# Kernel tuning notes

Hardware: AMD Instinct MI355X
Metric: run time of the kernel (lower is better)

## Reference

```python
import jax, jax.numpy as jnp
import numpy as np

B, N, K, C_IN, D = 4, 2048, 16, 480, 64
EPS = 1e-5


def _c1(x, w, b):
    # 1x1 Conv1d: x (B,C,N), w (O,C) -> (B,O,N)
    return jnp.einsum('oc,bcn->bon', w, x) + b[:, None]


def _c2(x, w, b):
    # 1x1 Conv2d: x (B,C,J,N), w (O,C) -> (B,O,J,N)
    return jnp.einsum('oc,bcjn->bojn', w, x) + b[:, None, None]


def _bn(x, g, b):
    # eval-mode BatchNorm2d with running_mean=0, running_var=1
    return x * (g / jnp.sqrt(1.0 + EPS))[:, None, None] + b[:, None, None]


def _mlp_res(x, w1, b1, w2, b2, ws, bs):
    return _c1(jax.nn.relu(_c1(x, w1, b1)), w2, b2) + _c1(x, ws, bs)


def _group(f, idx):
    # f (B,C,N), idx (B,K,N) int -> out[b,c,j,n] = f[b,c,idx[b,j,n]]  -> (B,C,K,N)
    return jax.vmap(lambda ff, ii: ff[:, ii])(f, idx)


def _knn_idx(xyz):
    # xyz (B,3,N) -> idx (B,K,N), excluding the self point (nearest neighbor)
    pts = xyz.transpose(0, 2, 1)  # (B,N,3)
    sq = jnp.sum(pts * pts, -1)
    d2 = sq[:, :, None] + sq[:, None, :] - 2.0 * jnp.einsum('bnd,bmd->bnm', pts, pts)
    _, idx = jax.lax.top_k(-d2, K + 1)  # (B,N,K+1), nearest first
    return idx.transpose(0, 2, 1)[:, 1:, :]  # drop self -> (B,K,N)


def _forward(idx, feature, xyz, bt1_w, bt1_b, bt2_w, bt2_b, bts_w, bts_b,
             q_w, q_b, k_w, k_b, v_w, v_b,
             fd1_w, fd1_b, fd_g, fd_bb, fd2_w, fd2_b,
             fg1_w, fg1_b, fg_g, fg_bb, fg2_w, fg2_b,
             at_w, at_b, m41_w, m41_b, m42_w, m42_b):
    x = _mlp_res(feature, bt1_w, bt1_b, bt2_w, bt2_b, bts_w, bts_b)  # (B,64,N)
    q = _c1(x, q_w, q_b)
    k = _c1(x, k_w, k_b)
    v = _c1(x, v_w, v_b)

    group_xyz = _group(xyz, idx)                       # (B,3,K,N)
    rel_xyz = xyz[:, :, None, :] - group_xyz           # (B,3,K,N)
    pos_enc = _c2(jax.nn.relu(_bn(_c2(rel_xyz, fd1_w, fd1_b), fd_g, fd_bb)), fd2_w, fd2_b)  # (B,64,K,N)

    k_local = _group(k, idx)                           # (B,64,K,N)
    v_local = _group(v, idx)
    qk_rel = q[:, :, None, :] - k_local
    attn = _c2(jax.nn.relu(_bn(_c2(qk_rel + pos_enc, fg1_w, fg1_b), fg_g, fg_bb)), fg2_w, fg2_b)  # (B,64,K,N)

    attn1 = attn.transpose(0, 1, 3, 2)                 # (B,64,N,K)
    # ConvTranspose2d(64,64,(4,1),(4,1)) with kernel==stride: out[b,o,4n+r,f] = sum_c x[b,c,n,f]*W[c,o,r] + bias[o]
    y = jnp.einsum('bcnf,cor->bonrf', attn1, at_w)
    y = y.reshape(y.shape[0], y.shape[1], -1, y.shape[4]) + at_b[None, :, None, None]  # (B,64,4N,K)
    attn = jax.nn.softmax(y, axis=1)

    value_rel = (v_local + pos_enc).transpose(0, 1, 3, 2)   # (B,64,N,K)
    value = jnp.repeat(value_rel, 4, axis=2)                # nearest upsample (4,1) -> (B,64,4N,K)

    res = jnp.einsum('bmnf,bmnf->bmn', attn, value)         # (B,64,4N)
    identity = jnp.repeat(x, 4, axis=2)                     # nearest upsample x4 -> (B,64,4N)
    res = res + identity
    completion = _c1(jax.nn.relu(_c1(res, m41_w, m41_b)), m42_w, m42_b)  # (B,3,4N)
    return completion, res


def setup_inputs() -> dict:
    key = jax.random.key(0)
    ks = jax.random.split(key, 24)
    i = iter(range(24))

    def w(shape):
        return (jax.random.normal(ks[next(i)], shape, dtype=jnp.float32) * 0.05)

    z = lambda n: jnp.zeros((n,), jnp.float32)
    o = lambda n: jnp.ones((n,), jnp.float32)
    return {
        'feature': jax.random.normal(ks[next(i)], (B, C_IN, N), dtype=jnp.float32),
        'xyz': jax.random.normal(ks[next(i)], (B, 3, N), dtype=jnp.float32),
        'bt1_w': w((D, C_IN)), 'bt1_b': z(D),
        'bt2_w': w((D, D)), 'bt2_b': z(D),
        'bts_w': w((D, C_IN)), 'bts_b': z(D),
        'q_w': w((D, D)), 'q_b': z(D),
        'k_w': w((D, D)), 'k_b': z(D),
        'v_w': w((D, D)), 'v_b': z(D),
        'fd1_w': w((D, 3)), 'fd1_b': z(D), 'fd_g': o(D), 'fd_bb': z(D),
        'fd2_w': w((D, D)), 'fd2_b': z(D),
        'fg1_w': w((4 * D, D)), 'fg1_b': z(4 * D), 'fg_g': o(4 * D), 'fg_bb': z(4 * D),
        'fg2_w': w((D, 4 * D)), 'fg2_b': z(D),
        'at_w': w((D, D, 4)), 'at_b': z(D),
        'm41_w': w((D, D)), 'm41_b': z(D),
        'm42_w': w((3, D)), 'm42_b': z(3),
    }


def reference(feature, xyz, bt1_w, bt1_b, bt2_w, bt2_b, bts_w, bts_b,
              q_w, q_b, k_w, k_b, v_w, v_b,
              fd1_w, fd1_b, fd_g, fd_bb, fd2_w, fd2_b,
              fg1_w, fg1_b, fg_g, fg_bb, fg2_w, fg2_b,
              at_w, at_b, m41_w, m41_b, m42_w, m42_b):
    idx = _knn_idx(xyz)
    return _forward(idx, feature, xyz, bt1_w, bt1_b, bt2_w, bt2_b, bts_w, bts_b,
                    q_w, q_b, k_w, k_b, v_w, v_b,
                    fd1_w, fd1_b, fd_g, fd_bb, fd2_w, fd2_b,
                    fg1_w, fg1_b, fg_g, fg_bb, fg2_w, fg2_b,
                    at_w, at_b, m41_w, m41_b, m42_w, m42_b)
```

## Files before the change

### kernel.cpp

```cpp
#include <hip/hip_runtime.h>

#define B_ 4
#define N_ 2048
#define K_ 16
#define CIN_ 480
#define UPN_ 8192
#define M_ (B_*N_*K_)
#define MX_ (B_*N_)
#define KCAP 448

typedef unsigned int u32;
typedef unsigned short u16;
typedef unsigned long long u64;
typedef __attribute__((ext_vector_type(8))) short short8;
typedef __attribute__((ext_vector_type(4))) float f32x4;

#define DEV static __device__ __forceinline__

DEV float b2f(u16 h){ return __uint_as_float(((u32)h)<<16); }
DEV u16 f2b(float f){
  u32 u = __float_as_uint(f);
  u32 r = u + 0x7fffu + ((u>>16)&1u);
  return (u16)(r>>16);
}
DEV u32 pack2(float a, float b){ return (u32)f2b(a) | ((u32)f2b(b)<<16); }
DEV bool detect_bf(const void* fg){ return ((((const u32*)fg)[0]) & 0xFFFFu) == 0x3F80u; }
DEV float ld(const void* p, int i, bool bf){
  return bf ? b2f(((const u16*)p)[i]) : ((const float*)p)[i];
}
DEV u64 makekey(float d2, int m){
  u32 bits = __float_as_uint(d2);
  bits = (bits & 0x80000000u) ? ~bits : (bits | 0x80000000u);
  return ((u64)bits<<32) | (u32)m;
}
DEV int swz64(int row, int colByte){ return row*128 + (colByte ^ ((row&7)<<4)); }
DEV int swzH (int row, int colByte){ return row*512 + (colByte ^ ((row&7)<<4)); }

__global__ __launch_bounds__(256) void convert_kernel(const void* __restrict__ xyz,
    const void* __restrict__ fg, float* __restrict__ fxyz)
{
  bool bf = detect_bf(fg);
  const int XT = B_*3*N_;
  for(int i = blockIdx.x*256+threadIdx.x; i < XT; i += gridDim.x*256)
    fxyz[i] = bf ? b2f(((const u16*)xyz)[i]) : ((const float*)xyz)[i];
}

__global__ __launch_bounds__(256) void transpose_kernel(const void* __restrict__ feature,
    const void* __restrict__ fg, u16* __restrict__ fxbT)
{
  __shared__ u16 s[32][34];
  bool bf = detect_bf(fg);
  int ntile = blockIdx.x, ctile = blockIdx.y, b = blockIdx.z;
  int tx = threadIdx.x & 31, ty = threadIdx.x >> 5;
  u64 base = (u64)b*CIN_*N_;
  #pragma unroll
  for(int r=0;r<4;r++){
    int c = ctile*32 + ty + r*8;
    int n = ntile*32 + tx;
    u64 i = base + (u64)c*N_ + n;
    s[ty + r*8][tx] = bf ? ((const u16*)feature)[i] : f2b(((const float*)feature)[i]);
  }
  __syncthreads();
  #pragma unroll
  for(int r=0;r<4;r++){
    int nl = ty + r*8;
    int n = ntile*32 + nl;
    fxbT[(u64)b*N_*CIN_ + (u64)n*CIN_ + ctile*32 + tx] = s[tx][nl];
  }
}

__global__ __launch_bounds__(256) void prep_kernel(
    const void* __restrict__ bt1_w, const void* __restrict__ bt1_b,
    const void* __restrict__ bt2_w, const void* __restrict__ bt2_b,
    const void* __restrict__ bts_w, const void* __restrict__ bts_b,
    const void* __restrict__ q_w, const void* __restrict__ q_b,
    const void* __restrict__ k_w, const void* __restrict__ k_b,
    const void* __restrict__ v_w, const void* __restrict__ v_b,
    const void* __restrict__ fd1_w, const void* __restrict__ fd1_b,
    const void* __restrict__ fd_g, const void* __restrict__ fd_bb,
    const void* __restrict__ fd2_w, const void* __restrict__ fd2_b,
    const void* __restrict__ fg1_w, const void* __restrict__ fg1_b,
    const void* __restrict__ fg_g, const void* __restrict__ fg_bb,
    const void* __restrict__ fg2_w, const void* __restrict__ fg2_b,
    const void* __restrict__ at_w, const void* __restrict__ at_b,
    const void* __restrict__ m41_w, const void* __restrict__ m41_b,
    const void* __restrict__ m42_w, const void* __restrict__ m42_b,
    float* __restrict__ W, u16* __restrict__ WB)
{
  int t = blockIdx.x*256 + threadIdx.x;
  bool bf = detect_bf(fd_g);
  const float inv = 0.9999950000374997f;
  if(t < 30720){ int c=t>>6, o=t&63; W[t] = ld(bt1_w,o*CIN_+c,bf); return; } t -= 30720;
  if(t < 30720){ int c=t>>6, o=t&63; W[30720+t] = ld(bts_w,o*CIN_+c,bf); return; } t -= 30720;
  if(t < 4096){ int c=t>>6, o=t&63; W[61440+t] = ld(bt2_w,o*64+c,bf); return; } t -= 4096;
  if(t < 4096){ int c=t>>6, o=t&63; W[65536+t] = ld(q_w,o*64+c,bf); return; } t -= 4096;
  if(t < 4096){ int c=t>>6, o=t&63; W[69632+t] = ld(k_w,o*64+c,bf); return; } t -= 4096;
  if(t < 4096){ int c=t>>6, o=t&63; W[73728+t] = ld(v_w,o*64+c,bf); return; } t -= 4096;
  if(t < 256){
    int o=t>>2, j=t&3; float s = ld(fd_g,o,bf)*inv;
    W[77824+t] = (j<3) ? s*ld(fd1_w,o*3+j,bf) : (s*ld(fd1_b,o,bf) + ld(fd_bb,o,bf));
    return;
  } t -= 256;
  if(t < 4096){ int o=t>>6, m=t&63; W[78080+t] = ld(fd2_w,m*64+o,bf); return; } t -= 4096;
  if(t < 16384){ int o=t>>6; float s=ld(fg_g,o,bf)*inv; W[82176+t] = s*ld(fg1_w,t,bf); return; } t -= 16384;
  if(t < 256){ float s=ld(fg_g,t,bf)*inv; W[98560+t] = s*ld(fg1_b,t,bf) + ld(fg_bb,t,bf); return; } t -= 256;
  if(t < 16384){ int o=t>>6, m=t&63; W[98816+t] = ld(fg2_w,m*256+o,bf); return; } t -= 16384;
  if(t < 16384){ int r=t>>12, rem=t&4095, o=rem>>6, c=rem&63;
                 W[115200+t] = ld(at_w,(c*64+o)*4+r,bf); return; } t -= 16384;
  if(t < 4096){ int m=t>>6, o=t&63; W[131584+t] = ld(m41_w,o*64+m,bf); return; } t -= 4096;
  if(t < 192){ W[135680+t] = ld(m42_w,t,bf); return; } t -= 192;
  if(t < 64){ W[135872+t] = ld(bt1_b,t,bf); return; } t -= 64;
  if(t < 64){ W[135936+t] = ld(bts_b,t,bf); return; } t -= 64;
  if(t < 64){ W[136000+t] = ld(bt2_b,t,bf); return; } t -= 64;
  if(t < 64){ W[136064+t] = ld(q_b,t,bf); return; } t -= 64;
  if(t < 64){ W[136128+t] = ld(k_b,t,bf); return; } t -= 64;
  if(t < 64){ W[136192+t] = ld(v_b,t,bf); return; } t -= 64;
  if(t < 64){ W[136256+t] = ld(fd2_b,t,bf); return; } t -= 64;
  if(t < 64){ W[136320+t] = ld(fg2_b,t,bf); return; } t -= 64;
  if(t < 64){ W[136384+t] = ld(at_b,t,bf); return; } t -= 64;
  if(t < 64){ W[136448+t] = ld(m41_b,t,bf); return; } t -= 64;
  if(t < 3){ W[136512+t] = ld(m42_b,t,bf); return; } t -= 3;
  if(t < 16384){ int o=t>>6; float s=ld(fg_g,o,bf)*inv; WB[t] = f2b(s*ld(fg1_w,t,bf)); return; } t -= 16384;
  if(t < 16384){ WB[16384+t] = f2b(ld(fg2_w,t,bf)); return; } t -= 16384;
  if(t < 16384){ int j=t>>6, c=t&63;
                 WB[32768+t] = f2b(ld(at_w,(c*64+(j&63))*4+(j>>6),bf)); return; } t -= 16384;
  if(t < 256){ W[136576+t] = ld(at_b,t&63,bf); return; } t -= 256;
  if(t < 4096){ WB[49152+t] = f2b(ld(fd2_w,t,bf)); return; } t -= 4096;
  if(t < 30720){ WB[53248+t] = f2b(ld(bt1_w,t,bf)); return; } t -= 30720;
  if(t < 30720){ WB[83968+t] = f2b(ld(bts_w,t,bf)); return; } t -= 30720;
  if(t < 4096){ WB[114688+t] = f2b(ld(bt2_w,t,bf)); return; } t -= 4096;
  if(t < 4096){ WB[118784+t] = f2b(ld(q_w,t,bf)); return; } t -= 4096;
  if(t < 4096){ WB[122880+t] = f2b(ld(k_w,t,bf)); return; } t -= 4096;
  if(t < 4096){ WB[126976+t] = f2b(ld(v_w,t,bf)); return; }
}

__global__ __launch_bounds__(256) void knn_kernel(const float* __restrict__ fxyz,
                                                  int* __restrict__ idx)
{
  __shared__ float px[N_], py[N_], pz[N_], sq[N_];
  __shared__ u64 sbuf[4][KCAP];
  __shared__ u64 smin[4][64];
  __shared__ int scnt[4][64];
  __shared__ u64 stau[4];
  int b = blockIdx.y;
  const float* xb = fxyz + (u64)b*3*N_;
  for(int i=threadIdx.x;i<N_;i+=256){
    float xx=xb[i], yy=xb[N_+i], zz=xb[2*N_+i];
    px[i]=xx; py[i]=yy; pz[i]=zz; sq[i]=xx*xx+yy*yy+zz*zz;
  }
  __syncthreads();
  int w = threadIdx.x>>6, l = threadIdx.x&63;
  int q = blockIdx.x*4 + w;
  float qx=px[q], qy=py[q], qz=pz[q], qs=sq[q];
  float d2c[32];
  u64 best=~0ull;
  #pragma unroll
  for(int j=0;j<32;j++){
    int m = l*32 + ((j+l)&31);
    float d2 = (qs+sq[m]) - 2.0f*(qx*px[m]+qy*py[m]+qz*pz[m]);
    d2c[j]=d2;
    u64 key = makekey(d2, m);
    best = key<best ? key : best;
  }
  smin[w][l]=best;
  __syncthreads();
  {
    int rank=0;
    for(int i=0;i<64;i++) rank += (smin[w][i] < best);
    if(rank==16) stau[w] = best;
  }
  __syncthreads();
  u64 tau = stau[w];
  int myc=0;
  #pragma unroll
  for(int j=0;j<32;j++){
    int m = l*32 + ((j+l)&31);
    myc += (makekey(d2c[j], m) <= tau);
  }
  scnt[w][l]=myc;
  __syncthreads();
  int off=0, tot=0;
  for(int i=0;i<64;i++){
    int c = scnt[w][i];
    tot += c;
    off += (i<l) ? c : 0;
  }
  #pragma unroll
  for(int j=0;j<32;j++){
    int m = l*32 + ((j+l)&31);
    u64 key = makekey(d2c[j], m);
    if(key<=tau && off<KCAP){ sbuf[w][off]=key; off++; }
  }
  __syncthreads();
  if(tot>KCAP) tot=KCAP;
  for(int p=l; p<tot; p+=64){
    u64 kk = sbuf[w][p];
    int rk=0;
    for(int i=0;i<tot;i++) rk += (sbuf[w][i] < kk);
    if(rk>=1 && rk<17) idx[(b*K_+(rk-1))*N_+q] = ((int)(kk & 0xffffffffu)) & (N_-1);
  }
}

__global__ __launch_bounds__(256) void gemm480_mfma(const u16* __restrict__ A,
    const u16* __restrict__ Wt, const float* __restrict__ bias,
    u16* __restrict__ hout, float* __restrict__ xsout)
{
  int tid=threadIdx.x, w=tid>>6, lane=tid&63;
  int rbase=(blockIdx.x*4+w)*64;
  int cbase=blockIdx.y*64;
  int lr=lane&15, lk=(lane>>4)*8;
  f32x4 acc[4][4];
  #pragma unroll
  for(int i=0;i<4;i++)
    #pragma unroll
    for(int j=0;j<4;j++) acc[i][j]=(f32x4){0.f,0.f,0.f,0.f};
  for(int kc=0;kc<CIN_;kc+=32){
    short8 a[4], bb[4];
    #pragma unroll
    for(int ti=0;ti<4;ti++)
      a[ti] = *(const short8*)(A + (u64)(rbase+ti*16+lr)*CIN_ + kc + lk);
    #pragma unroll
    for(int tj=0;tj<4;tj++)
      bb[tj] = *(const short8*)(Wt + (u64)(cbase+tj*16+lr)*CIN_ + kc + lk);
    #pragma unroll
    for(int ti=0;ti<4;ti++)
      #pragma unroll
      for(int tj=0;tj<4;tj++)
        acc[ti][tj] = __builtin_amdgcn_mfma_f32_16x16x32_bf16(a[ti], bb[tj], acc[ti][tj], 0,0,0);
  }
  int rq=(lane>>4)*4;
  #pragma unroll
  for(int ti=0;ti<4;ti++)
    #pragma unroll
    for(int tj=0;tj<4;tj++){
      int col = cbase + tj*16 + lr;
      float bv = bias[col];
      #pragma unroll
      for(int reg=0;reg<4;reg++){
        u64 row = rbase + ti*16 + rq + reg;
        float vv = acc[ti][tj][reg] + bv;
        if(blockIdx.y==0) hout[row*64 + col] = f2b(fmaxf(vv,0.f));
        else              xsout[row*64 + (col-64)] = vv;
      }
    }
}

__global__ __launch_bounds__(256) void x_mfma(const u16* __restrict__ A,
    const u16* __restrict__ Wt, const float* __restrict__ bias,
    const float* __restrict__ xs, float* __restrict__ x, u16* __restrict__ xb)
{
  int tid=threadIdx.x, w=tid>>6, lane=tid&63;
  int rbase=(blockIdx.x*4+w)*64;
  int lr=lane&15, lk=(lane>>4)*8;
  f32x4 acc[4][4];
  #pragma unroll
  for(int i=0;i<4;i++)
    #pragma unroll
    for(int j=0;j<4;j++) acc[i][j]=(f32x4){0.f,0.f,0.f,0.f};
  for(int kc=0;kc<64;kc+=32){
    short8 a[4], bb[4];
    #pragma unroll
    for(int ti=0;ti<4;ti++)
      a[ti] = *(const short8*)(A + (u64)(rbase+ti*16+lr)*64 + kc + lk);
    #pragma unroll
    for(int tj=0;tj<4;tj++)
      bb[tj] = *(const short8*)(Wt + (u64)(tj*16+lr)*64 + kc + lk);
    #pragma unroll
    for(int ti=0;ti<4;ti++)
      #pragma unroll
      for(int tj=0;tj<4;tj++)
        acc[ti][tj] = __builtin_amdgcn_mfma_f32_16x16x32_bf16(a[ti], bb[tj], acc[ti][tj], 0,0,0);
  }
  int rq=(lane>>4)*4;
  #pragma unroll
  for(int ti=0;ti<4;ti++)
    #pragma unroll
    for(int tj=0;tj<4;tj++){
      int col = tj*16 + lr;
      float bv = bias[col];
      #pragma unroll
      for(int reg=0;reg<4;reg++){
        u64 row = rbase + ti*16 + rq + reg;
        float vv = acc[ti][tj][reg] + bv + xs[row*64+col];
        x[row*64+col] = vv;
        xb[row*64+col] = f2b(vv);
      }
    }
}

__global__ __launch_bounds__(256) void qkv_mfma(const u16* __restrict__ A,
    const u16* __restrict__ Wt, const float* __restrict__ bias, float* __restrict__ qkv)
{
  int tid=threadIdx.x, w=tid>>6, lane=tid&63;
  int rbase=(blockIdx.x*4+w)*64;
  int cbase=blockIdx.y*64;
  int lr=lane&15, lk=(lane>>4)*8;
  f32x4 acc[4][4];
  #pragma unroll
  for(int i=0;i<4;i++)
    #pragma unroll
    for(int j=0;j<4;j++) acc[i][j]=(f32x4){0.f,0.f,0.f,0.f};
  for(int kc=0;kc<64;kc+=32){
    short8 a[4], bb[4];
    #pragma unroll
    for(int ti=0;ti<4;ti++)
      a[ti] = *(const short8*)(A + (u64)(rbase+ti*16+lr)*64 + kc + lk);
    #pragma unroll
    for(int tj=0;tj<4;tj++)
      bb[tj] = *(const short8*)(Wt + (u64)(cbase+tj*16+lr)*64 + kc + lk);
    #pragma unroll
    for(int ti=0;ti<4;ti++)
      #pragma unroll
      for(int tj=0;tj<4;tj++)
        acc[ti][tj] = __builtin_amdgcn_mfma_f32_16x16x32_bf16(a[ti], bb[tj], acc[ti][tj], 0,0,0);
  }
  int rq=(lane>>4)*4;
  #pragma unroll
  for(int ti=0;ti<4;ti++)
    #pragma unroll
    for(int tj=0;tj<4;tj++){
      int col = cbase + tj*16 + lr;
      float bv = bias[col];
      #pragma unroll
      for(int reg=0;reg<4;reg++){
        u64 row = rbase + ti*16 + rq + reg;
        qkv[row*192 + col] = acc[ti][tj][reg] + bv;
      }
    }
}

__global__ __launch_bounds__(256) void fused_chain(
    const int* __restrict__ idx, const float* __restrict__ fxyz,
    const float* __restrict__ qkv, const float* __restrict__ x,
    const float* __restrict__ fd1f,
    const u16* __restrict__ Wfd2, const float* __restrict__ bfd2,
    const u16* __restrict__ Wfg1, const float* __restrict__ bfg1,
    const u16* __restrict__ Wfg2, const float* __restrict__ bfg2,
    const u16* __restrict__ Wat,  const float* __restrict__ bat,
    const void* __restrict__ det, void* __restrict__ out)
{
  __shared__ alignas(16) unsigned char lds[49152];
  int tid = threadIdx.x;
  int w = tid>>6, lane = tid&63;
  int lr = lane&15, lk = (lane>>4)*8, rq = (lane>>4)*4;

  int erow = tid>>2, ecg = tid&3;
  int el = erow>>4, ef = erow&15;
  int bn_e = blockIdx.x*4 + el;
  int b_e = bn_e>>11, n_e = bn_e&(N_-1);
  int jn = idx[(b_e*K_+ef)*N_ + n_e] & (N_-1);

  {
    const float* xb = fxyz + (u64)b_e*3*N_;
    float rx = xb[n_e]      - xb[jn];
    float ry = xb[N_+n_e]   - xb[N_+jn];
    float rz = xb[2*N_+n_e] - xb[2*N_+jn];
    #pragma unroll
    for(int gg=0; gg<4; gg++){
      u64 pk=0;
      #pragma unroll
      for(int j=0;j<4;j++){
        f32x4 wv = *(const f32x4*)(fd1f + ((ecg*4+gg)*4+j)*4);
        float tv = fmaxf(wv[0]*rx + wv[1]*ry + wv[2]*rz + wv[3], 0.f);
        pk |= (u64)f2b(tv) << (16*j);
      }
      *(u64*)(lds + swz64(erow, (ecg*4+gg)*8)) = pk;
    }
  }
  __syncthreads();

  {
    f32x4 acc[4];
    #pragma unroll
    for(int i=0;i<4;i++) acc[i]=(f32x4){0.f,0.f,0.f,0.f};
    #pragma unroll
    for(int kc=0;kc<64;kc+=32){
      short8 wf = *(const short8*)(Wfd2 + (u64)(w*16+lr)*64 + kc + lk);
      #pragma unroll
      for(int ti=0;ti<4;ti++){
        short8 tf = *(const short8*)(lds + swz64(ti*16+lr, (kc+lk)*2));
        acc[ti] = __builtin_amdgcn_mfma_f32_16x16x32_bf16(wf, tf, acc[ti], 0,0,0);
      }
    }
    f32x4 b4 = *(const f32x4*)(bfd2 + w*16 + rq);
    #pragma unroll
    for(int ti=0;ti<4;ti++){
      u64 pk=0;
      #pragma unroll
      for(int reg=0;reg<4;reg++) pk |= (u64)f2b(acc[ti][reg] + b4[reg]) << (16*reg);
      *(u64*)(lds + 8192 + swz64(ti*16+lr, (w*16+rq)*2)) = pk;
    }
  }
  __syncthreads();

  {
    int mg = ecg*16;
    const float* qrow = qkv + (u64)(b_e*N_+n_e)*192 + mg;
    const float* krow = qkv + (u64)(b_e*N_+jn)*192 + 64 + mg;
    const float* vrow = qkv + (u64)(b_e*N_+jn)*192 + 128 + mg;
    #pragma unroll
    for(int g2=0; g2<4; g2++){
      f32x4 qv = *(const f32x4*)(qrow + g2*4);
      f32x4 kv = *(const f32x4*)(krow + g2*4);
      f32x4 vv = *(const f32x4*)(vrow + g2*4);
      int cb = (mg + g2*4)*2;
      u64 pw = *(const u64*)(lds + 8192 + swz64(erow, cb));
      u64 aw=0, vw=0;
      #pragma unroll
      for(int j=0;j<4;j++){
        float pv = b2f((u16)(pw>>(16*j)));
        aw |= (u64)f2b(qv[j] - kv[j] + pv) << (16*j);
        vw |= (u64)f2b(vv[j] + pv) << (16*j);
      }
      *(u64*)(lds + swz64(erow, cb)) = aw;
      *(u64*)(lds + 8192 + swz64(erow, cb)) = vw;
    }
  }
  __syncthreads();

  {
    f32x4 acc[4][4];
    #pragma unroll
    for(int i=0;i<4;i++)
      #pragma unroll
      for(int j=0;j<4;j++) acc[i][j]=(f32x4){0.f,0.f,0.f,0.f};
    #pragma unroll
    for(int kc=0;kc<64;kc+=32){
      short8 wf[4], af[4];
      #pragma unroll
      for(int ti=0;ti<4;ti++)
        wf[ti] = *(const short8*)(Wfg1 + (u64)(w*64+ti*16+lr)*64 + kc + lk);
      #pragma unroll
      for(int tj=0;tj<4;tj++)
        af[tj] = *(const short8*)(lds + swz64(tj*16+lr, (kc+lk)*2));
      #pragma unroll
      for(int ti=0;ti<4;ti++)
        #pragma unroll
        for(int tj=0;tj<4;tj++)
          acc[ti][tj] = __builtin_amdgcn_mfma_f32_16x16x32_bf16(wf[ti], af[tj], acc[ti][tj], 0,0,0);
    }
    #pragma unroll
    for(int ti=0;ti<4;ti++){
      f32x4 b4 = *(const f32x4*)(bfg1 + w*64 + ti*16 + rq);
      #pragma unroll
      for(int tj=0;tj<4;tj++){
        int rowh = tj*16 + lr;
        u64 pk=0;
        #pragma unroll
        for(int reg=0;reg<4;reg++)
          pk |= (u64)f2b(fmaxf(acc[ti][tj][reg] + b4[reg], 0.f)) << (16*reg);
        *(u64*)(lds + 16384 + swzH(rowh, (w*64+ti*16+rq)*2)) = pk;
      }
    }
  }
  __syncthreads();

  {
    f32x4 acc[4];
    #pragma unroll
    for(int i=0;i<4;i++) acc[i]=(f32x4){0.f,0.f,0.f,0.f};
    #pragma unroll
    for(int kc=0;kc<256;kc+=32){
      short8 wf = *(const short8*)(Wfg2 + (u64)(w*16+lr)*256 + kc + lk);
      #pragma unroll
      for(int ti=0;ti<4;ti++){
        short8 hf = *(const short8*)(lds + 16384 + swzH(ti*16+lr, (kc+lk)*2));
        acc[ti] = __builtin_amdgcn_mfma_f32_16x16x32_bf16(wf, hf, acc[ti], 0,0,0);
      }
    }
    f32x4 b4 = *(const f32x4*)(bfg2 + w*16 + rq);
    #pragma unroll
    for(int ti=0;ti<4;ti++){
      u64 pk=0;
      #pragma unroll
      for(int reg=0;reg<4;reg++) pk |= (u64)f2b(acc[ti][reg] + b4[reg]) << (16*reg);
      *(u64*)(lds + swz64(ti*16+lr, (w*16+rq)*2)) = pk;
    }
  }
  __syncthreads();

  {
    f32x4 acc[4][4];
    #pragma unroll
    for(int i=0;i<4;i++)
      #pragma unroll
      for(int j=0;j<4;j++) acc[i][j]=(f32x4){0.f,0.f,0.f,0.f};
    #pragma unroll
    for(int kc=0;kc<64;kc+=32){
      short8 wf[4], gf[4];
      #pragma unroll
      for(int ti=0;ti<4;ti++)
        wf[ti] = *(const short8*)(Wat + (u64)(w*64+ti*16+lr)*64 + kc + lk);
      #pragma unroll
      for(int tj=0;tj<4;tj++)
        gf[tj] = *(const short8*)(lds + swz64(tj*16+lr, (kc+lk)*2));
      #pragma unroll
      for(int ti=0;ti<4;ti++)
        #pragma unroll
        for(int tj=0;tj<4;tj++)
          acc[ti][tj] = __builtin_amdgcn_mfma_f32_16x16x32_bf16(wf[ti], gf[tj], acc[ti][tj], 0,0,0);
    }
    #pragma unroll
    for(int ti=0;ti<4;ti++){
      f32x4 b4 = *(const f32x4*)(bat + w*64 + ti*16 + rq);
      #pragma unroll
      for(int tj=0;tj<4;tj++){
        int rowy = tj*16 + lr;
        u64 pk=0;
        #pragma unroll
        for(int reg=0;reg<4;reg++)
          pk |= (u64)f2b(acc[ti][tj][reg] + b4[reg]) << (16*reg);
        *(u64*)(lds + 16384 + swzH(rowy, (w*64+ti*16+rq)*2)) = pk;
      }
    }
  }
  __syncthreads();

  int f = lane>>2, r = lane&3;
  int rowl = w*16 + f;
  float yv[64];
  #pragma unroll
  for(int j=0;j<8;j++){
    uint4 pk = *(const uint4*)(lds + 16384 + swzH(rowl, r*128 + j*16));
    yv[j*8+0]=__uint_as_float(pk.x<<16); yv[j*8+1]=__uint_as_float(pk.x&0xffff0000u);
    yv[j*8+2]=__uint_as_float(pk.y<<16); yv[j*8+3]=__uint_as_float(pk.y&0xffff0000u);
    yv[j*8+4]=__uint_as_float(pk.z<<16); yv[j*8+5]=__uint_as_float(pk.z&0xffff0000u);
    yv[j*8+6]=__uint_as_float(pk.w<<16); yv[j*8+7]=__uint_as_float(pk.w&0xffff0000u);
  }
  __syncthreads();

  float mx = yv[0];
  #pragma unroll
  for(int m=1;m<64;m++) mx = fmaxf(mx, yv[m]);
  float sm = 0.f;
  #pragma unroll
  for(int m=0;m<64;m++){ float e = __expf(yv[m]-mx); yv[m]=e; sm+=e; }
  float rinv = 1.0f/sm;
  #pragma unroll
  for(int j=0;j<8;j++){
    uint4 pk;
    pk.x = pack2(yv[j*8+0]*rinv, yv[j*8+1]*rinv);
    pk.y = pack2(yv[j*8+2]*rinv, yv[j*8+3]*rinv);
    pk.z = pack2(yv[j*8+4]*rinv, yv[j*8+5]*rinv);
    pk.w = pack2(yv[j*8+6]*rinv, yv[j*8+7]*rinv);
    *(uint4*)(lds + 16384 + swz64(tid, j*16)) = pk;
  }
  __syncthreads();

  int m = lane;
  float a0=0.f,a1=0.f,a2=0.f,a3=0.f;
  #pragma unroll
  for(int f2=0; f2<16; f2++){
    float vvf = b2f(*(const u16*)(lds + 8192 + swz64(w*16+f2, m*2)));
    int spr = w*64 + f2*4;
    a0 += b2f(*(const u16*)(lds + 16384 + swz64(spr+0, m*2))) * vvf;
    a1 += b2f(*(const u16*)(lds + 16384 + swz64(spr+1, m*2))) * vvf;
    a2 += b2f(*(const u16*)(lds + 16384 + swz64(spr+2, m*2))) * vvf;
    a3 += b2f(*(const u16*)(lds + 16384 + swz64(spr+3, m*2))) * vvf;
  }
  int bn = blockIdx.x*4 + w;
  int b = bn>>11, n = bn&(N_-1);
  float xv = x[(u64)bn*64 + m];
  u64 off = 98304 + ((u64)(b*64+m))*UPN_ + (u64)n*4;
  if(detect_bf(det)){
    u64 pk = (u64)f2b(a0+xv) | ((u64)f2b(a1+xv)<<16)
           | ((u64)f2b(a2+xv)<<32) | ((u64)f2b(a3+xv)<<48);
    *(u64*)((u16*)out + off) = pk;
  } else {
    f32x4 pk = {a0+xv, a1+xv, a2+xv, a3+xv};
    *(f32x4*)((float*)out + off) = pk;
  }
}

__global__ __launch_bounds__(256) void comp_kernel(
  const float* __restrict__ m41T, const float* __restrict__ m41b,
  const float* __restrict__ m42f, const float* __restrict__ m42b,
  const void* __restrict__ det, void* __restrict__ out)
{
  int t = blockIdx.x*256 + threadIdx.x;
  int un = t & (UPN_-1);
  int b = t >> 13;
  bool bf = detect_bf(det);
  float acc[64];
  #pragma unroll
  for(int o=0;o<64;o++) acc[o] = m41b[o];
  if(bf){
    const u16* rr = (const u16*)out + 98304 + (u64)b*64*UPN_ + un;
    for(int c=0;c<64;c++){
      float rv = b2f(rr[(u64)c*UPN_]);
      const float* w = m41T + c*64;
      #pragma unroll
      for(int o=0;o<64;o++) acc[o] += w[o]*rv;
    }
  } else {
    const float* rr = (const float*)out + 98304 + (u64)b*64*UPN_ + un;
    for(int c=0;c<64;c++){
      float rv = rr[(u64)c*UPN_];
      const float* w = m41T + c*64;
      #pragma unroll
      for(int o=0;o<64;o++) acc[o] += w[o]*rv;
    }
  }
  float c0=m42b[0], c1=m42b[1], c2=m42b[2];
  #pragma unroll
  for(int o=0;o<64;o++){
    float hv = fmaxf(acc[o],0.f);
    c0 += m42f[o]*hv; c1 += m42f[64+o]*hv; c2 += m42f[128+o]*hv;
  }
  u64 base = (u64)b*3*UPN_ + un;
  if(bf){
    u16* cp = (u16*)out;
    cp[base]=f2b(c0); cp[base+UPN_]=f2b(c1); cp[base+2*UPN_]=f2b(c2);
  } else {
    float* cp = (float*)out;
    cp[base]=c0; cp[base+UPN_]=c1; cp[base+2*UPN_]=c2;
  }
}

extern "C" void kernel_launch(void* const* d_in, const int* in_sizes, int n_in,
                              void* d_out, int out_size, void* d_ws, size_t ws_size,
                              hipStream_t stream)
{
  (void)in_sizes; (void)n_in; (void)out_size; (void)ws_size;
  const void* feature=d_in[0];
  const void* xyz   =d_in[1];
  const void* bt1_w =d_in[2];  const void* bt1_b=d_in[3];
  const void* bt2_w =d_in[4];  const void* bt2_b=d_in[5];
  const void* bts_w =d_in[6];  const void* bts_b=d_in[7];
  const void* q_w   =d_in[8];  const void* q_b =d_in[9];
  const void* k_w   =d_in[10]; const void* k_b =d_in[11];
  const void* v_w   =d_in[12]; const void* v_b =d_in[13];
  const void* fd1_w =d_in[14]; const void* fd1_b=d_in[15];
  const void* fd_g  =d_in[16]; const void* fd_bb=d_in[17];
  const void* fd2_w =d_in[18]; const void* fd2_b=d_in[19];
  const void* fg1_w =d_in[20]; const void* fg1_b=d_in[21];
  const void* fg_g  =d_in[22]; const void* fg_bb=d_in[23];
  const void* fg2_w =d_in[24]; const void* fg2_b=d_in[25];
  const void* at_w  =d_in[26]; const void* at_b =d_in[27];
  const void* m41_w =d_in[28]; const void* m41_b=d_in[29];
  const void* m42_w =d_in[30]; const void* m42_b=d_in[31];

  char* ws=(char*)d_ws;
  float* W   =(float*)(ws);
  u16*  WB   =(u16*)  (ws + 589824);
  int*  idx  =(int*)  (ws + 851968);
  float* x   =(float*)(ws + 1376256);
  float* qkv =(float*)(ws + 3473408);
  u16*  h    =(u16*)  (ws + 9764864);
  float* xs  =(float*)(ws + 10813440);
  u16*  xb   =(u16*)  (ws + 12910592);
  u16*  fxbT =(u16*)  (ws + 114622464);
  float* fxyz=(float*)(ws + 122486784);

  const float* W_fd1f = W+77824;
  const float* W_fg1fb= W+98560;
  const float* W_m41T = W+131584;
  const float* W_m42  = W+135680;
  const float* Wb_g480= W+135872;
  const float* Wb_bt2 = W+136000;
  const float* Wb_qkv = W+136064;
  const float* Wb_fd2 = W+136256;
  const float* Wb_fg2 = W+136320;
  const float* Wb_m41 = W+136448;
  const float* Wb_m42 = W+136512;
  const float* W_atb256 = W+136576;
  const u16* WB_fg1  = WB;
  const u16* WB_fg2  = WB+16384;
  const u16* WB_at   = WB+32768;
  const u16* WB_fd2  = WB+49152;
  const u16* WB_g480 = WB+53248;
  const u16* WB_bt2  = WB+114688;
  const u16* WB_qkv  = WB+118784;

  convert_kernel<<<96,256,0,stream>>>(xyz, fd_g, fxyz);
  prep_kernel<<<1047,256,0,stream>>>(bt1_w,bt1_b,bt2_w,bt2_b,bts_w,bts_b,q_w,q_b,k_w,k_b,
      v_w,v_b,fd1_w,fd1_b,fd_g,fd_bb,fd2_w,fd2_b,fg1_w,fg1_b,fg_g,fg_bb,fg2_w,fg2_b,
      at_w,at_b,m41_w,m41_b,m42_w,m42_b,W,WB);
  transpose_kernel<<<dim3(64,15,4),256,0,stream>>>(feature, fd_g, fxbT);
  knn_kernel<<<dim3(N_/4,B_),256,0,stream>>>(fxyz, idx);
  gemm480_mfma<<<dim3(MX_/256,2),256,0,stream>>>(fxbT, WB_g480, Wb_g480, h, xs);
  x_mfma<<<MX_/256,256,0,stream>>>(h, WB_bt2, Wb_bt2, xs, x, xb);
  qkv_mfma<<<dim3(MX_/256,3),256,0,stream>>>(xb, WB_qkv, Wb_qkv, qkv);
  fused_chain<<<B_*N_/4,256,0,stream>>>(idx, fxyz, qkv, x, W_fd1f,
      WB_fd2, Wb_fd2, WB_fg1, W_fg1fb, WB_fg2, Wb_fg2, WB_at, W_atb256, fd_g, d_out);
  comp_kernel<<<128,256,0,stream>>>(W_m41T, Wb_m41, W_m42, Wb_m42, fd_g, d_out);
}
```

Before: 279.3 us.

## Split hidden layer into halves, per-wave softmax, cut LDS, use hardware bf16 pack

```diff
diff --git a/kernel.cpp b/kernel.cpp
--- a/kernel.cpp
+++ b/kernel.cpp
@@ -17,13 +17,22 @@
 
 #define DEV static __device__ __forceinline__
 
+#define WAVE_WAIT() do{ asm volatile("s_waitcnt lgkmcnt(0)" ::: "memory"); \
+                        __builtin_amdgcn_sched_barrier(0); }while(0)
+
 DEV float b2f(u16 h){ return __uint_as_float(((u32)h)<<16); }
 DEV u16 f2b(float f){
   u32 u = __float_as_uint(f);
   u32 r = u + 0x7fffu + ((u>>16)&1u);
   return (u16)(r>>16);
 }
-DEV u32 pack2(float a, float b){ return (u32)f2b(a) | ((u32)f2b(b)<<16); }
+DEV u32 cvtpk(float a, float b){
+  u32 r; asm("v_cvt_pk_bf16_f32 %0, %1, %2" : "=v"(r) : "v"(a), "v"(b));
+  return r;
+}
+DEV u64 cvtpk4(float a, float b, float c, float d){
+  return (u64)cvtpk(a,b) | ((u64)cvtpk(c,d)<<32);
+}
 DEV bool detect_bf(const void* fg){ return ((((const u32*)fg)[0]) & 0xFFFFu) == 0x3F80u; }
 DEV float ld(const void* p, int i, bool bf){
   return bf ? b2f(((const u16*)p)[i]) : ((const float*)p)[i];
@@ -33,8 +42,8 @@
   bits = (bits & 0x80000000u) ? ~bits : (bits | 0x80000000u);
   return ((u64)bits<<32) | (u32)m;
 }
-DEV int swz64(int row, int colByte){ return row*128 + (colByte ^ ((row&7)<<4)); }
-DEV int swzH (int row, int colByte){ return row*512 + (colByte ^ ((row&7)<<4)); }
+DEV int swz64 (int row, int colByte){ return row*128 + (colByte ^ ((row&7)<<4)); }
+DEV int swz128(int row, int colByte){ return row*256 + (colByte ^ ((row&7)<<4)); }
 
 __global__ __launch_bounds__(256) void convert_kernel(const void* __restrict__ xyz,
     const void* __restrict__ fg, float* __restrict__ fxyz)
@@ -339,7 +348,7 @@
     const u16* __restrict__ Wat,  const float* __restrict__ bat,
     const void* __restrict__ det, void* __restrict__ out)
 {
-  __shared__ alignas(16) unsigned char lds[49152];
+  __shared__ alignas(16) unsigned char lds[32768];
   int tid = threadIdx.x;
   int w = tid>>6, lane = tid&63;
   int lr = lane&15, lk = (lane>>4)*8, rq = (lane>>4)*4;
@@ -357,14 +366,13 @@
     float rz = xb[2*N_+n_e] - xb[2*N_+jn];
     #pragma unroll
     for(int gg=0; gg<4; gg++){
-      u64 pk=0;
+      float tv[4];
       #pragma unroll
       for(int j=0;j<4;j++){
         f32x4 wv = *(const f32x4*)(fd1f + ((ecg*4+gg)*4+j)*4);
-        float tv = fmaxf(wv[0]*rx + wv[1]*ry + wv[2]*rz + wv[3], 0.f);
-        pk |= (u64)f2b(tv) << (16*j);
-      }
-      *(u64*)(lds + swz64(erow, (ecg*4+gg)*8)) = pk;
+        tv[j] = fmaxf(wv[0]*rx + wv[1]*ry + wv[2]*rz + wv[3], 0.f);
+      }
+      *(u64*)(lds + swz64(erow, (ecg*4+gg)*8)) = cvtpk4(tv[0],tv[1],tv[2],tv[3]);
     }
   }
   __syncthreads();
@@ -384,12 +392,9 @@
     }
     f32x4 b4 = *(const f32x4*)(bfd2 + w*16 + rq);
     #pragma unroll
-    for(int ti=0;ti<4;ti++){
-      u64 pk=0;
-      #pragma unroll
-      for(int reg=0;reg<4;reg++) pk |= (u64)f2b(acc[ti][reg] + b4[reg]) << (16*reg);
-      *(u64*)(lds + 8192 + swz64(ti*16+lr, (w*16+rq)*2)) = pk;
-    }
+    for(int ti=0;ti<4;ti++)
+      *(u64*)(lds + 8192 + swz64(ti*16+lr, (w*16+rq)*2)) =
+        cvtpk4(acc[ti][0]+b4[0], acc[ti][1]+b4[1], acc[ti][2]+b4[2], acc[ti][3]+b4[3]);
   }
   __syncthreads();
 
@@ -405,169 +410,135 @@
       f32x4 vv = *(const f32x4*)(vrow + g2*4);
       int cb = (mg + g2*4)*2;
       u64 pw = *(const u64*)(lds + 8192 + swz64(erow, cb));
-      u64 aw=0, vw=0;
-      #pragma unroll
-      for(int j=0;j<4;j++){
-        float pv = b2f((u16)(pw>>(16*j)));
-        aw |= (u64)f2b(qv[j] - kv[j] + pv) << (16*j);
-        vw |= (u64)f2b(vv[j] + pv) << (16*j);
-      }
-      *(u64*)(lds + swz64(erow, cb)) = aw;
-      *(u64*)(lds + 8192 + swz64(erow, cb)) = vw;
-    }
-  }
-  __syncthreads();
-
-  {
-    f32x4 acc[4][4];
-    #pragma unroll
-    for(int i=0;i<4;i++)
-      #pragma unroll
-      for(int j=0;j<4;j++) acc[i][j]=(f32x4){0.f,0.f,0.f,0.f};
-    #pragma unroll
-    for(int kc=0;kc<64;kc+=32){
-      short8 wf[4], af[4];
-      #pragma unroll
-      for(int ti=0;ti<4;ti++)
-        wf[ti] = *(const short8*)(Wfg1 + (u64)(w*64+ti*16+lr)*64 + kc + lk);
-      #pragma unroll
-      for(int tj=0;tj<4;tj++)
-        af[tj] = *(const short8*)(lds + swz64(tj*16+lr, (kc+lk)*2));
-      #pragma unroll
-      for(int ti=0;ti<4;ti++)
+      float p0=b2f((u16)pw), p1=b2f((u16)(pw>>16)), p2=b2f((u16)(pw>>32)), p3=b2f((u16)(pw>>48));
+      *(u64*)(lds + swz64(erow, cb)) =
+        cvtpk4(qv[0]-kv[0]+p0, qv[1]-kv[1]+p1, qv[2]-kv[2]+p2, qv[3]-kv[3]+p3);
+      *(u64*)(lds + 8192 + swz64(erow, cb)) =
+        cvtpk4(vv[0]+p0, vv[1]+p1, vv[2]+p2, vv[3]+p3);
+    }
+  }
+  __syncthreads();
+
+  float vreg[16];
+  #pragma unroll
+  for(int f2=0; f2<16; f2++)
+    vreg[f2] = b2f(*(const u16*)(lds + 8192 + swz64(w*16+f2, lane*2)));
+
+  f32x4 gacc[4];
+  #pragma unroll
+  for(int i=0;i<4;i++) gacc[i]=(f32x4){0.f,0.f,0.f,0.f};
+  #pragma unroll
+  for(int half=0; half<2; half++){
+    {
+      f32x4 hacc[2][4];
+      #pragma unroll
+      for(int i=0;i<2;i++)
+        #pragma unroll
+        for(int j=0;j<4;j++) hacc[i][j]=(f32x4){0.f,0.f,0.f,0.f};
+      #pragma unroll
+      for(int kc=0;kc<64;kc+=32){
+        short8 wf[2], af[4];
+        #pragma unroll
+        for(int ti=0;ti<2;ti++)
+          wf[ti] = *(const short8*)(Wfg1 + (u64)(half*128 + w*32 + ti*16 + lr)*64 + kc + lk);
         #pragma unroll
         for(int tj=0;tj<4;tj++)
-          acc[ti][tj] = __builtin_amdgcn_mfma_f32_16x16x32_bf16(wf[ti], af[tj], acc[ti][tj], 0,0,0);
-    }
-    #pragma unroll
-    for(int ti=0;ti<4;ti++){
-      f32x4 b4 = *(const f32x4*)(bfg1 + w*64 + ti*16 + rq);
+          af[tj] = *(const short8*)(lds + swz64(tj*16+lr, (kc+lk)*2));
+        #pragma unroll
+        for(int ti=0;ti<2;ti++)
+          #pragma unroll
+          for(int tj=0;tj<4;tj++)
+            hacc[ti][tj] = __builtin_amdgcn_mfma_f32_16x16x32_bf16(wf[ti], af[tj], hacc[ti][tj], 0,0,0);
+      }
+      #pragma unroll
+      for(int ti=0;ti<2;ti++){
+        f32x4 b4 = *(const f32x4*)(bfg1 + half*128 + w*32 + ti*16 + rq);
+        #pragma unroll
+        for(int tj=0;tj<4;tj++){
+          int row = tj*16 + lr;
+          *(u64*)(lds + 16384 + swz128(row, (w*32+ti*16+rq)*2)) =
+            cvtpk4(fmaxf(hacc[ti][tj][0]+b4[0],0.f), fmaxf(hacc[ti][tj][1]+b4[1],0.f),
+                   fmaxf(hacc[ti][tj][2]+b4[2],0.f), fmaxf(hacc[ti][tj][3]+b4[3],0.f));
+        }
+      }
+    }
+    __syncthreads();
+    #pragma unroll
+    for(int kc=0;kc<128;kc+=32){
+      short8 wf = *(const short8*)(Wfg2 + (u64)(w*16+lr)*256 + half*128 + kc + lk);
       #pragma unroll
       for(int tj=0;tj<4;tj++){
-        int rowh = tj*16 + lr;
-        u64 pk=0;
-        #pragma unroll
-        for(int reg=0;reg<4;reg++)
-          pk |= (u64)f2b(fmaxf(acc[ti][tj][reg] + b4[reg], 0.f)) << (16*reg);
-        *(u64*)(lds + 16384 + swzH(rowh, (w*64+ti*16+rq)*2)) = pk;
-      }
-    }
-  }
-  __syncthreads();
+        short8 hf = *(const short8*)(lds + 16384 + swz128(tj*16+lr, (kc+lk)*2));
+        gacc[tj] = __builtin_amdgcn_mfma_f32_16x16x32_bf16(wf, hf, gacc[tj], 0,0,0);
+      }
+    }
+    __syncthreads();
+  }
 
   {
+    f32x4 b4 = *(const f32x4*)(bfg2 + w*16 + rq);
+    #pragma unroll
+    for(int tj=0;tj<4;tj++)
+      *(u64*)(lds + swz64(tj*16+lr, (w*16+rq)*2)) =
+        cvtpk4(gacc[tj][0]+b4[0], gacc[tj][1]+b4[1], gacc[tj][2]+b4[2], gacc[tj][3]+b4[3]);
+  }
+  __syncthreads();
+
+  float aout[4];
+  unsigned char* Lp = lds + 16384 + w*2048;
+  #pragma unroll
+  for(int r=0;r<4;r++){
     f32x4 acc[4];
     #pragma unroll
     for(int i=0;i<4;i++) acc[i]=(f32x4){0.f,0.f,0.f,0.f};
     #pragma unroll
-    for(int kc=0;kc<256;kc+=32){
-      short8 wf = *(const short8*)(Wfg2 + (u64)(w*16+lr)*256 + kc + lk);
-      #pragma unroll
-      for(int ti=0;ti<4;ti++){
-        short8 hf = *(const short8*)(lds + 16384 + swzH(ti*16+lr, (kc+lk)*2));
-        acc[ti] = __builtin_amdgcn_mfma_f32_16x16x32_bf16(wf, hf, acc[ti], 0,0,0);
-      }
-    }
-    f32x4 b4 = *(const f32x4*)(bfg2 + w*16 + rq);
-    #pragma unroll
-    for(int ti=0;ti<4;ti++){
-      u64 pk=0;
-      #pragma unroll
-      for(int reg=0;reg<4;reg++) pk |= (u64)f2b(acc[ti][reg] + b4[reg]) << (16*reg);
-      *(u64*)(lds + swz64(ti*16+lr, (w*16+rq)*2)) = pk;
-    }
-  }
-  __syncthreads();
-
-  {
-    f32x4 acc[4][4];
-    #pragma unroll
-    for(int i=0;i<4;i++)
-      #pragma unroll
-      for(int j=0;j<4;j++) acc[i][j]=(f32x4){0.f,0.f,0.f,0.f};
-    #pragma unroll
     for(int kc=0;kc<64;kc+=32){
-      short8 wf[4], gf[4];
-      #pragma unroll
-      for(int ti=0;ti<4;ti++)
-        wf[ti] = *(const short8*)(Wat + (u64)(w*64+ti*16+lr)*64 + kc + lk);
-      #pragma unroll
-      for(int tj=0;tj<4;tj++)
-        gf[tj] = *(const short8*)(lds + swz64(tj*16+lr, (kc+lk)*2));
-      #pragma unroll
-      for(int ti=0;ti<4;ti++)
-        #pragma unroll
-        for(int tj=0;tj<4;tj++)
-          acc[ti][tj] = __builtin_amdgcn_mfma_f32_16x16x32_bf16(wf[ti], gf[tj], acc[ti][tj], 0,0,0);
-    }
-    #pragma unroll
-    for(int ti=0;ti<4;ti++){
-      f32x4 b4 = *(const f32x4*)(bat + w*64 + ti*16 + rq);
-      #pragma unroll
-      for(int tj=0;tj<4;tj++){
-        int rowy = tj*16 + lr;
-        u64 pk=0;
-        #pragma unroll
-        for(int reg=0;reg<4;reg++)
-          pk |= (u64)f2b(acc[ti][tj][reg] + b4[reg]) << (16*reg);
-        *(u64*)(lds + 16384 + swzH(rowy, (w*64+ti*16+rq)*2)) = pk;
-      }
-    }
-  }
-  __syncthreads();
-
-  int f = lane>>2, r = lane&3;
-  int rowl = w*16 + f;
-  float yv[64];
-  #pragma unroll
-  for(int j=0;j<8;j++){
-    uint4 pk = *(const uint4*)(lds + 16384 + swzH(rowl, r*128 + j*16));
-    yv[j*8+0]=__uint_as_float(pk.x<<16); yv[j*8+1]=__uint_as_float(pk.x&0xffff0000u);
-    yv[j*8+2]=__uint_as_float(pk.y<<16); yv[j*8+3]=__uint_as_float(pk.y&0xffff0000u);
-    yv[j*8+4]=__uint_as_float(pk.z<<16); yv[j*8+5]=__uint_as_float(pk.z&0xffff0000u);
-    yv[j*8+6]=__uint_as_float(pk.w<<16); yv[j*8+7]=__uint_as_float(pk.w&0xffff0000u);
-  }
-  __syncthreads();
-
-  float mx = yv[0];
-  #pragma unroll
-  for(int m=1;m<64;m++) mx = fmaxf(mx, yv[m]);
-  float sm = 0.f;
-  #pragma unroll
-  for(int m=0;m<64;m++){ float e = __expf(yv[m]-mx); yv[m]=e; sm+=e; }
-  float rinv = 1.0f/sm;
-  #pragma unroll
-  for(int j=0;j<8;j++){
-    uint4 pk;
-    pk.x = pack2(yv[j*8+0]*rinv, yv[j*8+1]*rinv);
-    pk.y = pack2(yv[j*8+2]*rinv, yv[j*8+3]*rinv);
-    pk.z = pack2(yv[j*8+4]*rinv, yv[j*8+5]*rinv);
-    pk.w = pack2(yv[j*8+6]*rinv, yv[j*8+7]*rinv);
-    *(uint4*)(lds + 16384 + swz64(tid, j*16)) = pk;
-  }
-  __syncthreads();
-
-  int m = lane;
-  float a0=0.f,a1=0.f,a2=0.f,a3=0.f;
-  #pragma unroll
-  for(int f2=0; f2<16; f2++){
-    float vvf = b2f(*(const u16*)(lds + 8192 + swz64(w*16+f2, m*2)));
-    int spr = w*64 + f2*4;
-    a0 += b2f(*(const u16*)(lds + 16384 + swz64(spr+0, m*2))) * vvf;
-    a1 += b2f(*(const u16*)(lds + 16384 + swz64(spr+1, m*2))) * vvf;
-    a2 += b2f(*(const u16*)(lds + 16384 + swz64(spr+2, m*2))) * vvf;
-    a3 += b2f(*(const u16*)(lds + 16384 + swz64(spr+3, m*2))) * vvf;
-  }
+      short8 gf = *(const short8*)(lds + swz64(w*16+lr, (kc+lk)*2));
+      #pragma unroll
+      for(int ct=0;ct<4;ct++){
+        short8 wf = *(const short8*)(Wat + (u64)(r*64 + ct*16 + lr)*64 + kc + lk);
+        acc[ct] = __builtin_amdgcn_mfma_f32_16x16x32_bf16(wf, gf, acc[ct], 0,0,0);
+      }
+    }
+    float yv[16];
+    #pragma unroll
+    for(int ct=0;ct<4;ct++){
+      f32x4 b4 = *(const f32x4*)(bat + r*64 + ct*16 + rq);
+      #pragma unroll
+      for(int reg=0;reg<4;reg++) yv[ct*4+reg] = acc[ct][reg] + b4[reg];
+    }
+    float mx = yv[0];
+    #pragma unroll
+    for(int m=1;m<16;m++) mx = fmaxf(mx, yv[m]);
+    mx = fmaxf(mx, __shfl_xor(mx, 16));
+    mx = fmaxf(mx, __shfl_xor(mx, 32));
+    float sm = 0.f;
+    #pragma unroll
+    for(int m=0;m<16;m++){ float e = __expf(yv[m]-mx); yv[m]=e; sm+=e; }
+    sm += __shfl_xor(sm, 16);
+    sm += __shfl_xor(sm, 32);
+    float rinv = 1.0f/sm;
+    #pragma unroll
+    for(int ct=0;ct<4;ct++)
+      *(u64*)(Lp + swz64(lr, (ct*16+rq)*2)) =
+        cvtpk4(yv[ct*4+0]*rinv, yv[ct*4+1]*rinv, yv[ct*4+2]*rinv, yv[ct*4+3]*rinv);
+    WAVE_WAIT();
+    float a = 0.f;
+    #pragma unroll
+    for(int f2=0; f2<16; f2++)
+      a += b2f(*(const u16*)(Lp + swz64(f2, lane*2))) * vreg[f2];
+    aout[r] = a;
+    WAVE_WAIT();
+  }
+
   int bn = blockIdx.x*4 + w;
   int b = bn>>11, n = bn&(N_-1);
-  float xv = x[(u64)bn*64 + m];
-  u64 off = 98304 + ((u64)(b*64+m))*UPN_ + (u64)n*4;
+  float xv = x[(u64)bn*64 + lane];
+  u64 off = 98304 + ((u64)(b*64+lane))*UPN_ + (u64)n*4;
   if(detect_bf(det)){
-    u64 pk = (u64)f2b(a0+xv) | ((u64)f2b(a1+xv)<<16)
-           | ((u64)f2b(a2+xv)<<32) | ((u64)f2b(a3+xv)<<48);
-    *(u64*)((u16*)out + off) = pk;
+    *(u64*)((u16*)out + off) = cvtpk4(aout[0]+xv, aout[1]+xv, aout[2]+xv, aout[3]+xv);
   } else {
-    f32x4 pk = {a0+xv, a1+xv, a2+xv, a3+xv};
+    f32x4 pk = {aout[0]+xv, aout[1]+xv, aout[2]+xv, aout[3]+xv};
     *(f32x4*)((float*)out + off) = pk;
   }
 }
```

After: 296.7 us. +6.2%, slower.
